# Performance work log

Measured on AMD Instinct MI355X. Metric: run time of the kernel, lower is better.

## Reference

```python
import math
import jax, jax.numpy as jnp
import numpy as np

G = 96       # grid side; N = G*G tokens, one token per grid cell
D = 512      # d_model
R = 2        # radius (Chebyshev)
LN_EPS = 1e-5

# 24 neighbor offsets in the (2R+1)^2 window, excluding (0,0) (self is excluded in the torch code)
_OFF = np.array([(dx, dy) for dx in range(-R, R + 1) for dy in range(-R, R + 1) if not (dx == 0 and dy == 0)], dtype=np.int32)


def _layer_norm(x, g, b):
    m = jnp.mean(x, axis=-1, keepdims=True)
    v = jnp.mean(jnp.square(x - m), axis=-1, keepdims=True)
    return (x - m) * jax.lax.rsqrt(v + LN_EPS) * g + b


def setup_inputs() -> dict:
    key = jax.random.key(0)
    ks = jax.random.split(key, 12)
    N = G * G
    x = jax.random.normal(ks[0], (N, D), jnp.float32)
    gx, gy = jnp.meshgrid(jnp.arange(G), jnp.arange(G), indexing='ij')
    grid = jnp.stack([gx.ravel(), gy.ravel()], axis=-1).astype(jnp.int32)  # [N,2], one token per cell

    def lin(k, din, dout):
        return jax.random.normal(k, (din, dout), jnp.float32) * (1.0 / math.sqrt(din))

    return {
        'x': x, 'grid': grid,
        'Wq': lin(ks[1], D, D), 'bq': jnp.zeros((D,), jnp.float32),
        'Wk': lin(ks[2], D, D), 'bk': jnp.zeros((D,), jnp.float32),
        'Wv': lin(ks[3], D, D), 'bv': jnp.zeros((D,), jnp.float32),
        'Wo': lin(ks[4], D, D), 'bo': jnp.zeros((D,), jnp.float32),
        'g1': jnp.ones((D,), jnp.float32), 'b1': jnp.zeros((D,), jnp.float32),
        'g2': jnp.ones((D,), jnp.float32), 'b2': jnp.zeros((D,), jnp.float32),
        'W1': lin(ks[5], D, 4 * D), 'bf1': jnp.zeros((4 * D,), jnp.float32),
        'W2': lin(ks[6], 4 * D, D), 'bf2': jnp.zeros((D,), jnp.float32),
    }


def reference(x, grid, Wq, bq, Wk, bk, Wv, bv, Wo, bo, g1, b1, g2, b2, W1, bf1, W2, bf2):
    # dropout is identity (eval mode)
    h = _layer_norm(x, g1, b1)
    q = h @ Wq + bq
    k = h @ Wk + bk
    v = h @ Wv + bv

    off = jnp.asarray(_OFF)                      # [K=24, 2]
    nx = grid[:, 0:1] + off[None, :, 0]          # [N, K]
    ny = grid[:, 1:2] + off[None, :, 1]
    valid = (nx >= 0) & (nx < G) & (ny >= 0) & (ny < G)
    idx = jnp.where(valid, nx * G + ny, 0)       # row-major cell -> token index

    k_nbr = k[idx]                               # [N, K, D]
    v_nbr = v[idx]                               # [N, K, D]
    scores = jnp.einsum('nd,nkd->nk', q, k_nbr) / math.sqrt(D)
    neg = jnp.finfo(scores.dtype).min
    scores = jnp.where(valid, scores, neg)
    attn = jax.nn.softmax(scores, axis=-1)       # every token has >=8 valid neighbors for G>R
    out = jnp.einsum('nk,nkd->nd', attn, v_nbr)  # [N, D]

    x = x + out @ Wo + bo
    h2 = _layer_norm(x, g2, b2)
    ffn = jax.nn.gelu(h2 @ W1 + bf1, approximate=False) @ W2 + bf2
    return x + ffn
```

## Files before the change

kernel.cpp:

```cpp
#include <hip/hip_runtime.h>

typedef unsigned short u16;
typedef unsigned int u32;
typedef __bf16 bf16x8 __attribute__((ext_vector_type(8)));
typedef float f32x4 __attribute__((ext_vector_type(4)));

#define GRID_G 96
#define DMODEL 512
#define NTOK (GRID_G * GRID_G)

__device__ __forceinline__ u16 f2bf(float f) {
  u32 u = __builtin_bit_cast(u32, f);
  u += 0x7fffu + ((u >> 16) & 1u);
  return (u16)(u >> 16);
}
__device__ __forceinline__ void unpack8(uint4 u, float* f) {
  f[0] = __builtin_bit_cast(float, u.x << 16);
  f[1] = __builtin_bit_cast(float, u.x & 0xffff0000u);
  f[2] = __builtin_bit_cast(float, u.y << 16);
  f[3] = __builtin_bit_cast(float, u.y & 0xffff0000u);
  f[4] = __builtin_bit_cast(float, u.z << 16);
  f[5] = __builtin_bit_cast(float, u.z & 0xffff0000u);
  f[6] = __builtin_bit_cast(float, u.w << 16);
  f[7] = __builtin_bit_cast(float, u.w & 0xffff0000u);
}
__device__ __forceinline__ float gelu_fast(float x) {
  float y = 0.7978845608f * (x + 0.044715f * x * x * x);
  float a = fabsf(y);
  float e = __expf(-2.0f * a);
  float th = (1.0f - e) / (1.0f + e);
  th = __builtin_copysignf(th, y);
  return 0.5f * x * (1.0f + th);
}

__global__ __launch_bounds__(256) void k_transpose_bf16(
    const float* __restrict__ src, u16* __restrict__ dst, int R, int C) {
  __shared__ float tile[32][33];
  int bx = blockIdx.x * 32, by = blockIdx.y * 32;
  int tx = threadIdx.x & 31, ty = threadIdx.x >> 5;
#pragma unroll
  for (int i = 0; i < 4; ++i) {
    int r = ty + i * 8;
    tile[r][tx] = src[(size_t)(by + r) * C + (bx + tx)];
  }
  __syncthreads();
#pragma unroll
  for (int i = 0; i < 4; ++i) {
    int c = ty + i * 8;
    dst[(size_t)(bx + c) * R + (by + tx)] = f2bf(tile[tx][c]);
  }
}

__global__ __launch_bounds__(256) void k_transpose4(
    const float* __restrict__ s0, const float* __restrict__ s1,
    const float* __restrict__ s2, const float* __restrict__ s3,
    u16* __restrict__ d0, u16* __restrict__ d1,
    u16* __restrict__ d2, u16* __restrict__ d3) {
  __shared__ float tile[32][33];
  const float* src = blockIdx.z == 0 ? s0 : blockIdx.z == 1 ? s1 : blockIdx.z == 2 ? s2 : s3;
  u16* dst = blockIdx.z == 0 ? d0 : blockIdx.z == 1 ? d1 : blockIdx.z == 2 ? d2 : d3;
  int bx = blockIdx.x * 32, by = blockIdx.y * 32;
  int tx = threadIdx.x & 31, ty = threadIdx.x >> 5;
#pragma unroll
  for (int i = 0; i < 4; ++i) {
    int r = ty + i * 8;
    tile[r][tx] = src[(size_t)(by + r) * 512 + (bx + tx)];
  }
  __syncthreads();
#pragma unroll
  for (int i = 0; i < 4; ++i) {
    int c = ty + i * 8;
    dst[(size_t)(bx + c) * 512 + (by + tx)] = f2bf(tile[tx][c]);
  }
}

__global__ __launch_bounds__(256) void k_concat3(
    const float* __restrict__ a, const float* __restrict__ b,
    const float* __restrict__ c, float* __restrict__ o) {
  int i = blockIdx.x * 256 + threadIdx.x;
  if (i < 512) o[i] = a[i];
  else if (i < 1024) o[i] = b[i - 512];
  else o[i] = c[i - 1024];
}

__global__ __launch_bounds__(256) void k_layernorm_bf16(
    const float* __restrict__ x, const float* __restrict__ g,
    const float* __restrict__ b, u16* __restrict__ out) {
  int tid = threadIdx.x, wid = tid >> 6, lane = tid & 63;
  int row = blockIdx.x * 4 + wid;
  const float* xr = x + (size_t)row * DMODEL;
  float4 v0 = *(const float4*)(xr + lane * 4);
  float4 v1 = *(const float4*)(xr + 256 + lane * 4);
  float s = v0.x + v0.y + v0.z + v0.w + v1.x + v1.y + v1.z + v1.w;
  float sq = v0.x * v0.x + v0.y * v0.y + v0.z * v0.z + v0.w * v0.w +
             v1.x * v1.x + v1.y * v1.y + v1.z * v1.z + v1.w * v1.w;
#pragma unroll
  for (int m = 1; m < 64; m <<= 1) {
    s += __shfl_xor(s, m);
    sq += __shfl_xor(sq, m);
  }
  float mean = s * (1.0f / DMODEL);
  float rstd = rsqrtf(sq * (1.0f / DMODEL) - mean * mean + 1e-5f);
  float4 ga = *(const float4*)(g + lane * 4);
  float4 gb = *(const float4*)(g + 256 + lane * 4);
  float4 ba = *(const float4*)(b + lane * 4);
  float4 bb = *(const float4*)(b + 256 + lane * 4);
  ushort4 o0, o1;
  o0.x = f2bf((v0.x - mean) * rstd * ga.x + ba.x);
  o0.y = f2bf((v0.y - mean) * rstd * ga.y + ba.y);
  o0.z = f2bf((v0.z - mean) * rstd * ga.z + ba.z);
  o0.w = f2bf((v0.w - mean) * rstd * ga.w + ba.w);
  o1.x = f2bf((v1.x - mean) * rstd * gb.x + bb.x);
  o1.y = f2bf((v1.y - mean) * rstd * gb.y + bb.y);
  o1.z = f2bf((v1.z - mean) * rstd * gb.z + bb.z);
  o1.w = f2bf((v1.w - mean) * rstd * gb.w + bb.w);
  u16* op = out + (size_t)row * DMODEL;
  *(ushort4*)(op + lane * 4) = o0;
  *(ushort4*)(op + 256 + lane * 4) = o1;
}

__global__ __launch_bounds__(256) void k_attn(
    const u16* __restrict__ q, const u16* __restrict__ kk,
    const u16* __restrict__ vv, const int* __restrict__ gpos,
    u16* __restrict__ out) {
  int tid = threadIdx.x, wid = tid >> 6, lane = tid & 63;
  int n = blockIdx.x * 4 + wid;
  int px = gpos[2 * n], py = gpos[2 * n + 1];
  float qf[8];
  unpack8(*(const uint4*)(q + (size_t)n * DMODEL + lane * 8), qf);
  float sc[24];
  int nid[24];
  bool ok[24];
#pragma unroll
  for (int j = 0; j < 24; ++j) {
    int jj = j < 12 ? j : j + 1;
    int dx = jj / 5 - 2, dy = jj % 5 - 2;
    int nx = px + dx, ny = py + dy;
    bool val = (nx >= 0) && (nx < GRID_G) && (ny >= 0) && (ny < GRID_G);
    int id = val ? nx * GRID_G + ny : 0;
    ok[j] = val;
    nid[j] = id;
    float kf[8];
    unpack8(*(const uint4*)(kk + (size_t)id * DMODEL + lane * 8), kf);
    float p = 0.f;
#pragma unroll
    for (int e = 0; e < 8; ++e) p += qf[e] * kf[e];
#pragma unroll
    for (int m = 1; m < 64; m <<= 1) p += __shfl_xor(p, m);
    sc[j] = p * 0.04419417382415922f;
  }
  float mx = -3.0e38f;
#pragma unroll
  for (int j = 0; j < 24; ++j)
    if (ok[j]) mx = fmaxf(mx, sc[j]);
  float wsum = 0.f, w[24];
#pragma unroll
  for (int j = 0; j < 24; ++j) {
    w[j] = ok[j] ? expf(sc[j] - mx) : 0.f;
    wsum += w[j];
  }
  float inv = 1.0f / wsum;
  float acc[8] = {0, 0, 0, 0, 0, 0, 0, 0};
#pragma unroll
  for (int j = 0; j < 24; ++j) {
    float vf[8];
    unpack8(*(const uint4*)(vv + (size_t)nid[j] * DMODEL + lane * 8), vf);
    float wj = w[j];
#pragma unroll
    for (int e = 0; e < 8; ++e) acc[e] += wj * vf[e];
  }
  uint4 o;
  o.x = (u32)f2bf(acc[0] * inv) | ((u32)f2bf(acc[1] * inv) << 16);
  o.y = (u32)f2bf(acc[2] * inv) | ((u32)f2bf(acc[3] * inv) << 16);
  o.z = (u32)f2bf(acc[4] * inv) | ((u32)f2bf(acc[5] * inv) << 16);
  o.w = (u32)f2bf(acc[6] * inv) | ((u32)f2bf(acc[7] * inv) << 16);
  *(uint4*)(out + (size_t)n * DMODEL + lane * 8) = o;
}

template <int EPI>
__global__ __launch_bounds__(256, 2) void k_gemm(
    const u16* __restrict__ A, const u16* __restrict__ Bt,
    const float* __restrict__ bias, const float* __restrict__ res,
    float* __restrict__ outF, u16* __restrict__ outB,
    int M, int N, int K, int tiles_n) {
  __shared__ u16 lds[32768];
  const int t = threadIdx.x, wid = t >> 6, lane = t & 63;
  const int nwg = gridDim.x, bid = blockIdx.x;
  const int l = ((bid & 7) * (nwg >> 3)) + (bid >> 3);
  const int bM = (l / tiles_n) * 128, bN = (l % tiles_n) * 128;
  const int wr = wid >> 1, wc = wid & 1, lr = lane & 15, lg = lane >> 4;

  const int rs = lane >> 3;
  const int cl = (lane & 7) ^ rs;
  const u16* gA[4];
  const u16* gB[4];
  int dstL[4];
#pragma unroll
  for (int j = 0; j < 4; ++j) {
    int r = wid * 32 + j * 8 + rs;
    gA[j] = A + (size_t)(bM + r) * K + cl * 8;
    gB[j] = Bt + (size_t)(bN + r) * K + cl * 8;
    dstL[j] = wid * 2048 + j * 512;
  }

#define STAGE(BUF, KOFF)                                                              \
  {                                                                                   \
    _Pragma("unroll") for (int j = 0; j < 4; ++j) {                                   \
      __builtin_amdgcn_global_load_lds(                                               \
          (const __attribute__((address_space(1))) void*)(gA[j] + (KOFF)),            \
          (__attribute__((address_space(3))) void*)(lds + (BUF)*16384 + dstL[j]),     \
          16, 0, 0);                                                                  \
      __builtin_amdgcn_global_load_lds(                                               \
          (const __attribute__((address_space(1))) void*)(gB[j] + (KOFF)),            \
          (__attribute__((address_space(3))) void*)(lds + (BUF)*16384 + 8192 + dstL[j]), \
          16, 0, 0);                                                                  \
    }                                                                                 \
  }

  const int offA0 = (wr * 64 + lr) * 64 + ((0 + lg) ^ (lr & 7)) * 8;
  const int offA1 = (wr * 64 + lr) * 64 + ((4 + lg) ^ (lr & 7)) * 8;
  const int offB0 = (wc * 64 + lr) * 64 + ((0 + lg) ^ (lr & 7)) * 8;
  const int offB1 = (wc * 64 + lr) * 64 + ((4 + lg) ^ (lr & 7)) * 8;

  f32x4 acc[4][4];
#pragma unroll
  for (int i = 0; i < 4; ++i)
#pragma unroll
    for (int j = 0; j < 4; ++j) acc[i][j] = (f32x4){0.f, 0.f, 0.f, 0.f};

#define COMPUTE(BUF)                                                                  \
  {                                                                                   \
    _Pragma("unroll") for (int ks = 0; ks < 2; ++ks) {                                \
      const int oa = (BUF)*16384 + (ks ? offA1 : offA0);                              \
      const int ob = (BUF)*16384 + 8192 + (ks ? offB1 : offB0);                       \
      bf16x8 af[4], bfr[4];                                                           \
      _Pragma("unroll") for (int mt = 0; mt < 4; ++mt)                                \
          af[mt] = __builtin_bit_cast(bf16x8, *(const uint4*)(lds + oa + mt * 1024)); \
      _Pragma("unroll") for (int nt = 0; nt < 4; ++nt)                                \
          bfr[nt] = __builtin_bit_cast(bf16x8, *(const uint4*)(lds + ob + nt * 1024));\
      _Pragma("unroll") for (int mt = 0; mt < 4; ++mt)                                \
          _Pragma("unroll") for (int nt = 0; nt < 4; ++nt)                            \
              acc[mt][nt] = __builtin_amdgcn_mfma_f32_16x16x32_bf16(                  \
                  af[mt], bfr[nt], acc[mt][nt], 0, 0, 0);                             \
    }                                                                                 \
  }

  const int nk = K >> 6;
  STAGE(0, 0);
  __syncthreads();
  int koff = 64;
  for (int tt = 0; tt < nk; tt += 2) {
    if (tt + 1 < nk) STAGE(1, koff);
    COMPUTE(0);
    __syncthreads();
    if (tt + 2 < nk) STAGE(0, koff + 64);
    COMPUTE(1);
    __syncthreads();
    koff += 128;
  }
#undef STAGE
#undef COMPUTE

#pragma unroll
  for (int mt = 0; mt < 4; ++mt) {
#pragma unroll
    for (int nt = 0; nt < 4; ++nt) {
      int col = bN + wc * 64 + nt * 16 + lr;
      float bc = bias[col];
      int row0 = bM + wr * 64 + mt * 16 + lg * 4;
#pragma unroll
      for (int r = 0; r < 4; ++r) {
        float val = acc[mt][nt][r] + bc;
        if constexpr (EPI == 1) {
          size_t off = (size_t)(row0 + r) * N + col;
          outF[off] = res[off] + val;
        } else if constexpr (EPI == 2) {
          size_t off = (size_t)(row0 + r) * N + col;
          outB[off] = f2bf(gelu_fast(val));
        } else {
          int seg = col >> 9;
          size_t off = (size_t)seg * ((size_t)NTOK * DMODEL) +
                       (size_t)(row0 + r) * DMODEL + (col & 511);
          outB[off] = f2bf(val);
        }
      }
    }
  }
}

extern "C" void kernel_launch(void* const* d_in, const int* in_sizes, int n_in,
                              void* d_out, int out_size, void* d_ws, size_t ws_size,
                              hipStream_t stream) {
  const float* x = (const float*)d_in[0];
  const int* gpos = (const int*)d_in[1];
  const float* Wq = (const float*)d_in[2];
  const float* bq = (const float*)d_in[3];
  const float* Wk = (const float*)d_in[4];
  const float* bk = (const float*)d_in[5];
  const float* Wv = (const float*)d_in[6];
  const float* bv = (const float*)d_in[7];
  const float* Wo = (const float*)d_in[8];
  const float* bo = (const float*)d_in[9];
  const float* g1 = (const float*)d_in[10];
  const float* b1 = (const float*)d_in[11];
  const float* g2 = (const float*)d_in[12];
  const float* b2 = (const float*)d_in[13];
  const float* W1 = (const float*)d_in[14];
  const float* bf1 = (const float*)d_in[15];
  const float* W2 = (const float*)d_in[16];
  const float* bf2 = (const float*)d_in[17];
  float* out = (float*)d_out;
  char* ws = (char*)d_ws;

  constexpr size_t SZ_W512 = (size_t)512 * 512 * 2;
  constexpr size_t SZ_W2048 = (size_t)512 * 2048 * 2;
  constexpr size_t SZ_ACT = (size_t)NTOK * 512 * 2;

  u16* WQT = (u16*)(ws + 0);
  u16* WKT = (u16*)(ws + SZ_W512);
  u16* WVT = (u16*)(ws + 2 * SZ_W512);
  u16* WOT = (u16*)(ws + 3 * SZ_W512);
  u16* W1T = (u16*)(ws + 4 * SZ_W512);
  u16* W2T = (u16*)(ws + 4 * SZ_W512 + SZ_W2048);
  float* BCAT = (float*)(ws + 4 * SZ_W512 + 2 * SZ_W2048);
  char* actbase = ws + 4 * SZ_W512 + 2 * SZ_W2048 + 6144;
  u16* H = (u16*)(actbase);
  u16* Q = (u16*)(actbase + SZ_ACT);
  u16* KB = (u16*)(actbase + 2 * SZ_ACT);
  u16* VB = (u16*)(actbase + 3 * SZ_ACT);
  u16* H2 = (u16*)(actbase + 4 * SZ_ACT);
  u16* U = (u16*)(actbase);

  k_transpose4<<<dim3(16, 16, 4), 256, 0, stream>>>(Wq, Wk, Wv, Wo, WQT, WKT, WVT, WOT);
  k_transpose_bf16<<<dim3(64, 16), 256, 0, stream>>>(W1, W1T, 512, 2048);
  k_transpose_bf16<<<dim3(16, 64), 256, 0, stream>>>(W2, W2T, 2048, 512);
  k_concat3<<<6, 256, 0, stream>>>(bq, bk, bv, BCAT);

  k_layernorm_bf16<<<NTOK / 4, 256, 0, stream>>>(x, g1, b1, H);

  k_gemm<3><<<864, 256, 0, stream>>>(H, WQT, BCAT, nullptr, nullptr, Q, NTOK, 1536, 512, 12);

  k_attn<<<NTOK / 4, 256, 0, stream>>>(Q, KB, VB, gpos, H);

  k_gemm<1><<<288, 256, 0, stream>>>(H, WOT, bo, x, out, nullptr, NTOK, 512, 512, 4);

  k_layernorm_bf16<<<NTOK / 4, 256, 0, stream>>>(out, g2, b2, H2);

  k_gemm<2><<<1152, 256, 0, stream>>>(H2, W1T, bf1, nullptr, nullptr, U, NTOK, 2048, 512, 16);

  k_gemm<1><<<288, 256, 0, stream>>>(U, W2T, bf2, out, out, nullptr, NTOK, 512, 2048, 4);
}
```

Before: 168.0 us.

## Add 256x256-tile 8-wave GEMM with direct-to-LDS loads for QKV and FFN1

Adds a new GEMM kernel using 256x256 output tiles with 512 threads, global_load_lds direct-to-LDS staging, XOR-swizzled LDS layout, a double-buffered phased schedule interleaving prefetch with MFMA bursts, and an XCD-aware block remap. It replaces the 128x128-tile GEMM for the QKV projection and the first FFN layer, aiming to raise arithmetic intensity and overlap loads with compute. The tradeoff is fewer blocks (216/288) on a device with 256 CUs, which may leave tail imbalance, plus 128KB of LDS per block and heavy register use. The old kernel's epilogue is simplified to cover only the remaining residual path.

```diff
diff --git a/kernel.cpp b/kernel.cpp
--- a/kernel.cpp
+++ b/kernel.cpp
@@ -271,17 +271,137 @@
 #pragma unroll
       for (int r = 0; r < 4; ++r) {
         float val = acc[mt][nt][r] + bc;
+        size_t off = (size_t)(row0 + r) * N + col;
         if constexpr (EPI == 1) {
-          size_t off = (size_t)(row0 + r) * N + col;
           outF[off] = res[off] + val;
-        } else if constexpr (EPI == 2) {
-          size_t off = (size_t)(row0 + r) * N + col;
-          outB[off] = f2bf(gelu_fast(val));
         } else {
-          int seg = col >> 9;
-          size_t off = (size_t)seg * ((size_t)NTOK * DMODEL) +
-                       (size_t)(row0 + r) * DMODEL + (col & 511);
           outB[off] = f2bf(val);
+        }
+      }
+    }
+  }
+}
+
+#define BARR { __builtin_amdgcn_s_barrier(); __builtin_amdgcn_sched_barrier(0); }
+#define WAITV0 asm volatile("s_waitcnt vmcnt(0)" ::: "memory");
+#define WAITV2 asm volatile("s_waitcnt vmcnt(2)" ::: "memory");
+#define WAITV4 asm volatile("s_waitcnt vmcnt(4)" ::: "memory");
+
+template <int EPI>
+__global__ __launch_bounds__(512, 2) void k_gemm_big(
+    const u16* __restrict__ A, const u16* __restrict__ Bt,
+    const float* __restrict__ bias, u16* __restrict__ outB,
+    int K, int N, int tiles_n) {
+  __shared__ u16 lds[65536];
+  const int t = threadIdx.x, wid = t >> 6, lane = t & 63;
+  const int wr = wid >> 2, wc = wid & 3;
+  const int lr = lane & 15, lg = lane >> 4;
+  const int nwg = gridDim.x, bid = blockIdx.x;
+  const int qq = nwg >> 3, rr = nwg & 7;
+  const int xcd = bid & 7, seq = bid >> 3;
+  const int l = (xcd < rr ? xcd * (qq + 1) : rr * (qq + 1) + (xcd - rr) * qq) + seq;
+  const int bM = (l / tiles_n) * 256, bN = (l % tiles_n) * 256;
+
+  const int srow = wid * 8 + (lane >> 3);
+  const int cl = (lane & 7) ^ (lane >> 3);
+  const u16* pA = A + (size_t)(bM + srow) * K + cl * 8;
+  const u16* pB = Bt + (size_t)(bN + srow) * K + cl * 8;
+  const int dbase = wid * 512;
+
+#define STG(C, BOFF, PTR, H, KT)                                                       \
+  { _Pragma("unroll") for (int j = 0; j < 2; ++j)                                      \
+      __builtin_amdgcn_global_load_lds(                                                \
+        (const __attribute__((address_space(1))) void*)((PTR) + (size_t)((H)*128 + j*64) * K + (KT)), \
+        (__attribute__((address_space(3))) void*)(lds + (C)*32768 + (BOFF) + (H)*8192 + dbase + j*4096), \
+        16, 0, 0); }
+
+  const int swz0 = ((0 + lg) ^ (lr & 7)) * 8;
+  const int swz1 = ((4 + lg) ^ (lr & 7)) * 8;
+
+  f32x4 acc[4][2][4];
+#pragma unroll
+  for (int q = 0; q < 4; ++q)
+#pragma unroll
+    for (int u = 0; u < 2; ++u)
+#pragma unroll
+      for (int nt = 0; nt < 4; ++nt) acc[q][u][nt] = (f32x4){0.f, 0.f, 0.f, 0.f};
+
+  bf16x8 b[4][2], a[2][2];
+
+#define PH_READ_B(C)                                                                   \
+  { _Pragma("unroll") for (int nt = 0; nt < 4; ++nt) {                                 \
+      const u16* bb = lds + (C)*32768 + 16384 + (wc * 64 + nt * 16 + lr) * 64;         \
+      b[nt][0] = __builtin_bit_cast(bf16x8, *(const uint4*)(bb + swz0));               \
+      b[nt][1] = __builtin_bit_cast(bf16x8, *(const uint4*)(bb + swz1)); } }
+
+#define PH_READ_A(C, Q)                                                                \
+  { _Pragma("unroll") for (int u = 0; u < 2; ++u) {                                    \
+      const u16* ab = lds + (C)*32768 + ((Q)*64 + wr * 32 + u * 16 + lr) * 64;         \
+      a[u][0] = __builtin_bit_cast(bf16x8, *(const uint4*)(ab + swz0));                \
+      a[u][1] = __builtin_bit_cast(bf16x8, *(const uint4*)(ab + swz1)); } }
+
+#define PH_MFMA(Q)                                                                     \
+  { __builtin_amdgcn_s_setprio(1);                                                     \
+    _Pragma("unroll") for (int u = 0; u < 2; ++u)                                      \
+    _Pragma("unroll") for (int nt = 0; nt < 4; ++nt) {                                 \
+      acc[Q][u][nt] = __builtin_amdgcn_mfma_f32_16x16x32_bf16(a[u][0], b[nt][0], acc[Q][u][nt], 0, 0, 0); \
+      acc[Q][u][nt] = __builtin_amdgcn_mfma_f32_16x16x32_bf16(a[u][1], b[nt][1], acc[Q][u][nt], 0, 0, 0); } \
+    __builtin_amdgcn_s_setprio(0); }
+
+#define TILE_BODY(TT, C)                                                               \
+  {                                                                                    \
+    const bool pre = (TT) + 1 < nk;                                                    \
+    const int kn = ((TT) + 1) << 6;                                                    \
+    PH_READ_B(C); PH_READ_A(C, 0);                                                     \
+    if (pre) STG(C ^ 1, 16384, pB, 0, kn);                                             \
+    BARR; PH_MFMA(0); BARR;                                                            \
+    PH_READ_A(C, 1);                                                                   \
+    if (pre) { STG(C ^ 1, 16384, pB, 1, kn); WAITV4; } else { WAITV0; }                \
+    BARR; PH_MFMA(1); BARR;                                                            \
+    PH_READ_A(C, 2);                                                                   \
+    if (pre) STG(C ^ 1, 0, pA, 0, kn);                                                 \
+    BARR; PH_MFMA(2); BARR;                                                            \
+    PH_READ_A(C, 3);                                                                   \
+    if (pre) { STG(C ^ 1, 0, pA, 1, kn); WAITV2; }                                     \
+    BARR; PH_MFMA(3); BARR;                                                            \
+  }
+
+  STG(0, 16384, pB, 0, 0); STG(0, 16384, pB, 1, 0);
+  STG(0, 0, pA, 0, 0);     STG(0, 0, pA, 1, 0);
+  WAITV0;
+  BARR;
+
+  const int nk = K >> 6;
+  for (int tt = 0; tt < nk; tt += 2) {
+    TILE_BODY(tt, 0);
+    TILE_BODY(tt + 1, 1);
+  }
+#undef TILE_BODY
+#undef PH_MFMA
+#undef PH_READ_A
+#undef PH_READ_B
+#undef STG
+
+#pragma unroll
+  for (int q = 0; q < 4; ++q) {
+#pragma unroll
+    for (int u = 0; u < 2; ++u) {
+#pragma unroll
+      for (int nt = 0; nt < 4; ++nt) {
+        int col = bN + wc * 64 + nt * 16 + lr;
+        float bc = bias[col];
+        int row0 = bM + q * 64 + wr * 32 + u * 16 + lg * 4;
+#pragma unroll
+        for (int r = 0; r < 4; ++r) {
+          float val = acc[q][u][nt][r] + bc;
+          if constexpr (EPI == 2) {
+            outB[(size_t)(row0 + r) * N + col] = f2bf(gelu_fast(val));
+          } else {
+            int seg = col >> 9;
+            size_t off = (size_t)seg * ((size_t)NTOK * DMODEL) +
+                         (size_t)(row0 + r) * DMODEL + (col & 511);
+            outB[off] = f2bf(val);
+          }
         }
       }
     }
@@ -338,7 +458,7 @@
 
   k_layernorm_bf16<<<NTOK / 4, 256, 0, stream>>>(x, g1, b1, H);
 
-  k_gemm<3><<<864, 256, 0, stream>>>(H, WQT, BCAT, nullptr, nullptr, Q, NTOK, 1536, 512, 12);
+  k_gemm_big<3><<<216, 512, 0, stream>>>(H, WQT, BCAT, Q, 512, 1536, 6);
 
   k_attn<<<NTOK / 4, 256, 0, stream>>>(Q, KB, VB, gpos, H);
 
@@ -346,7 +466,7 @@
 
   k_layernorm_bf16<<<NTOK / 4, 256, 0, stream>>>(out, g2, b2, H2);
 
-  k_gemm<2><<<1152, 256, 0, stream>>>(H2, W1T, bf1, nullptr, nullptr, U, NTOK, 2048, 512, 16);
+  k_gemm_big<2><<<288, 512, 0, stream>>>(H2, W1T, bf1, U, 512, 2048, 8);
 
   k_gemm<1><<<288, 256, 0, stream>>>(U, W2T, bf2, out, out, nullptr, NTOK, 512, 2048, 4);
 }
```

Result: slower. 181.3 us (+7.9%).
